# Performance work log

Measured on AMD Instinct MI355X. Metric: run time of the kernel, lower is better.

The kernel has to match this reference:

```python
import jax, jax.numpy as jnp
import numpy as np

B, D, H, L = 2, 1024, 16, 4
BLK = 16                 # block_size == max_text_tokens
MT, MF = 16, 2032        # max_text_tokens, max_font_tokens
S = MT + MF              # 2048
NB = S // BLK            # 128 blocks
V = 490                  # font_vocab_size
HD = D // H              # 64
WIN = 30                 # 3*max_glyph_tokens/block_size = 3*160/16
NGLOB, NRAND = 1, 2      # BigBird global / random blocks
SOS = 0.42


def _make_layout():
    # Deterministic BigBird block layout per head: [H, NB, NB] bool
    rng = np.random.default_rng(0)
    layout = np.zeros((H, NB, NB), dtype=bool)
    layout[:, :NGLOB, :] = True          # global rows
    layout[:, :, :NGLOB] = True          # global cols
    for i in range(NB):                  # sliding window
        layout[:, i, max(0, i - WIN // 2):min(NB, i + WIN // 2 + 1)] = True
    for h in range(H):                   # random blocks
        for i in range(NB):
            layout[h, i, rng.choice(NB, size=NRAND, replace=False)] = True
    return jnp.asarray(layout)


def setup_inputs() -> dict:
    key = jax.random.key(0)
    ks = jax.random.split(key, 16)
    p = lambda k, shape: (0.02 * jax.random.normal(k, shape)).astype(jnp.float32)
    return {
        "text_embeddings": jax.random.normal(ks[0], (B, MT, D), jnp.float32),
        "font_embeddings": jax.random.normal(ks[1], (B, MF, D), jnp.float32),
        "layout": _make_layout(),
        "Wq": p(ks[2], (L, D, D)), "bq": jnp.zeros((L, D), jnp.float32),
        "Wk": p(ks[3], (L, D, D)), "bk": jnp.zeros((L, D), jnp.float32),
        "Wv": p(ks[4], (L, D, D)), "bv": jnp.zeros((L, D), jnp.float32),
        "Wo": p(ks[5], (L, D, D)), "bo": jnp.zeros((L, D), jnp.float32),
        "ln1_g": jnp.ones((L, D), jnp.float32), "ln1_b": jnp.zeros((L, D), jnp.float32),
        "ln2_g": jnp.ones((L, D), jnp.float32), "ln2_b": jnp.zeros((L, D), jnp.float32),
        "W1": p(ks[6], (L, D, 4 * D)), "b1": jnp.zeros((L, 4 * D), jnp.float32),
        "W2": p(ks[7], (L, 4 * D, D)), "b2": jnp.zeros((L, D), jnp.float32),
        "lnf_g": jnp.ones((D,), jnp.float32), "lnf_b": jnp.zeros((D,), jnp.float32),
        "Wout": p(ks[8], (D, V)),
    }


def _ln(x, g, b, eps=1e-5):
    mu = x.mean(-1, keepdims=True)
    var = ((x - mu) ** 2).mean(-1, keepdims=True)
    return (x - mu) * jax.lax.rsqrt(var + eps) * g + b


def _forward(text_embeddings, font_embeddings, layout, Wq, bq, Wk, bk, Wv, bv, Wo, bo,
             ln1_g, ln1_b, ln2_g, ln2_b, W1, b1, W2, b2, lnf_g, lnf_b, Wout):
    sos = jnp.full((B, 1, D), SOS, text_embeddings.dtype)
    x = jnp.concatenate([sos, text_embeddings, font_embeddings[:, :-1, :]], axis=1)  # [B,S,D]
    # token-level mask = block-sparse BigBird layout AND causal -> [H,S,S]
    tok_mask = jnp.repeat(jnp.repeat(layout, BLK, axis=1), BLK, axis=2)
    tok_mask = tok_mask & jnp.tril(jnp.ones((S, S), bool))[None]
    neg = jnp.asarray(-1e9, x.dtype)
    scale = jnp.asarray(1.0 / np.sqrt(HD), x.dtype)

    def layer(x, p):
        wq, bq_, wk, bk_, wv, bv_, wo, bo_, g1, gb1, g2, gb2, w1, bb1, w2, bb2 = p
        q = (x @ wq + bq_).reshape(B, S, H, HD).transpose(0, 2, 1, 3)
        k = (x @ wk + bk_).reshape(B, S, H, HD).transpose(0, 2, 1, 3)
        v = (x @ wv + bv_).reshape(B, S, H, HD).transpose(0, 2, 1, 3)
        scores = jnp.einsum('bhqd,bhkd->bhqk', q, k) * scale
        scores = jnp.where(tok_mask[None], scores, neg)
        probs = jax.nn.softmax(scores, axis=-1)
        a = jnp.einsum('bhqk,bhkd->bhqd', probs, v).transpose(0, 2, 1, 3).reshape(B, S, D)
        a = a @ wo + bo_
        x = _ln(x + a, g1, gb1)                                   # post-norm residual
        m = jax.nn.gelu(x @ w1 + bb1, approximate=False) @ w2 + bb2  # dropout=eval no-op
        x = _ln(x + m, g2, gb2)
        return x, None

    params = (Wq, bq, Wk, bk, Wv, bv, Wo, bo, ln1_g, ln1_b, ln2_g, ln2_b, W1, b1, W2, b2)
    x, _ = jax.lax.scan(jax.checkpoint(layer), x, params)
    logits = _ln(x, lnf_g, lnf_b) @ Wout                          # [B,S,V]
    return logits[:, :MT, :], logits[:, MT:, :]


def reference(text_embeddings, font_embeddings, layout, Wq, bq, Wk, bk, Wv, bv, Wo, bo,
              ln1_g, ln1_b, ln2_g, ln2_b, W1, b1, W2, b2, lnf_g, lnf_b, Wout):
    return _forward(text_embeddings, font_embeddings, layout, Wq, bq, Wk, bk, Wv, bv, Wo, bo,
                    ln1_g, ln1_b, ln2_g, ln2_b, W1, b1, W2, b2, lnf_g, lnf_b, Wout)
```

## Files before the change

### kernel.cpp

```cpp
#include <hip/hip_runtime.h>
#include <hip/hip_bf16.h>
#include <math.h>


typedef __hip_bfloat16 bf16;
typedef __attribute__((ext_vector_type(8))) short bf16x8;
typedef __attribute__((ext_vector_type(8))) unsigned short us8;
typedef __attribute__((ext_vector_type(4))) unsigned short us4;
typedef __attribute__((ext_vector_type(4))) float f32x4;
typedef __attribute__((ext_vector_type(8))) _Float16 f16x8;

#define S_LEN 2048
#define D_MODEL 1024
#define NBLK 128
#define NHEAD 16
#define BATCH 2
#define M_ROWS 4096
#define VOCAB 490

__device__ __forceinline__ float ldw(const void* p, size_t i, bool bf) {
    return bf ? __bfloat162float(((const bf16*)p)[i]) : ((const float*)p)[i];
}
__device__ __forceinline__ bool is_bf(const unsigned* probe) {
    return probe[0] != 0x3F800000u;
}
__device__ __forceinline__ unsigned short f2b(float f) {
    union { float f; unsigned u; } x; x.f = f;
    return (unsigned short)((x.u + 0x7FFFu + ((x.u >> 16) & 1u)) >> 16);
}
__device__ __forceinline__ unsigned short f2h(float f) {
    union { _Float16 h; unsigned short u; } x; x.h = (_Float16)f;
    return x.u;
}
__device__ __forceinline__ unsigned packh(float a, float b) {
    return (unsigned)f2h(a) | ((unsigned)f2h(b) << 16);
}

__global__ __launch_bounds__(256) void norm_layout_kernel(
    const unsigned char* __restrict__ lraw, unsigned char* __restrict__ mask)
{
    int i = blockIdx.x * 256 + threadIdx.x;
    bool bytes_mode = (lraw[1] == 1);
    unsigned char v;
    if (bytes_mode) v = lraw[i] ? 1 : 0;
    else            v = ((const unsigned*)lraw)[i] ? 1 : 0;
    mask[i] = v;
}

__global__ __launch_bounds__(256) void build_x_kernel(
    const void* __restrict__ text, const void* __restrict__ font,
    float* __restrict__ x, unsigned short* __restrict__ xb,
    const unsigned* __restrict__ probe)
{
    bool bf = is_bf(probe);
    size_t idx = (size_t)blockIdx.x * 256 + threadIdx.x;
    int d = (int)(idx & 1023);
    int s = (int)((idx >> 10) & 2047);
    int b = (int)(idx >> 21);
    float v;
    if (s == 0)       v = bf ? 0.419921875f : 0.42f;
    else if (s <= 16) v = ldw(text, ((size_t)(b * 16 + (s - 1))) * 1024 + d, bf);
    else              v = ldw(font, ((size_t)(b * 2032 + (s - 17))) * 1024 + d, bf);
    x[idx] = v;
    xb[idx] = f2b(v);
}

__global__ __launch_bounds__(256) void transw_kernel(
    const void* __restrict__ W, size_t wOff, unsigned short* __restrict__ Wt,
    int K, int N, const unsigned* __restrict__ probe)
{
    bool bf = is_bf(probe);
    __shared__ unsigned short tile[32][34];
    int k0 = blockIdx.x * 32, n0 = blockIdx.y * 32;
    int t = threadIdx.x, c = t & 31, r0 = t >> 5;
    #pragma unroll
    for (int i = 0; i < 4; ++i) {
        int n = n0 + c;
        float v = (n < N) ? ldw(W, wOff + (size_t)(k0 + r0 + i * 8) * N + n, bf) : 0.f;
        tile[r0 + i * 8][c] = f2b(v);
    }
    __syncthreads();
    #pragma unroll
    for (int i = 0; i < 4; ++i)
        Wt[(size_t)(n0 + r0 + i * 8) * K + k0 + c] = tile[c][r0 + i * 8];
}

__global__ __launch_bounds__(256) void transw4_kernel(
    const void* __restrict__ Wa, const void* __restrict__ Wb,
    const void* __restrict__ Wc, const void* __restrict__ Wd,
    size_t wOff, unsigned short* __restrict__ wt,
    const unsigned* __restrict__ probe)
{
    bool bf = is_bf(probe);
    int z = blockIdx.z;
    const void* W = z == 0 ? Wa : (z == 1 ? Wb : (z == 2 ? Wc : Wd));
    unsigned short* Wt = wt + (size_t)z * (1u << 20);
    __shared__ unsigned short tile[32][34];
    int k0 = blockIdx.x * 32, n0 = blockIdx.y * 32;
    int t = threadIdx.x, c = t & 31, r0 = t >> 5;
    #pragma unroll
    for (int i = 0; i < 4; ++i) {
        float v = ldw(W, wOff + (size_t)(k0 + r0 + i * 8) * 1024 + n0 + c, bf);
        tile[r0 + i * 8][c] = f2b(v);
    }
    __syncthreads();
    #pragma unroll
    for (int i = 0; i < 4; ++i)
        Wt[(size_t)(n0 + r0 + i * 8) * 1024 + k0 + c] = tile[c][r0 + i * 8];
}

__global__ __launch_bounds__(512) void gemm_kernel(
    const unsigned short* __restrict__ Ab,
    const unsigned short* __restrict__ Wt, size_t wtStride,
    const void* __restrict__ b0, const void* __restrict__ b1p, const void* __restrict__ b2p,
    size_t bOff,
    float* __restrict__ C0, float* __restrict__ C1, float* __restrict__ C2,
    void* __restrict__ Cb0, void* __restrict__ Cb1, void* __restrict__ Cb2,
    int M, int N, int K, int act, int outmode, const unsigned* __restrict__ probe)
{
    bool bf = is_bf(probe);
    __shared__ __align__(16) unsigned short As[2][128 * 64];
    __shared__ __align__(16) unsigned short Bs[2][128 * 64];

    int t    = threadIdx.x;
    int lane = t & 63;
    int wid  = t >> 6;
    int wm   = wid >> 2;
    int wn   = wid & 3;

    int gx  = gridDim.x;
    int nwg = gx * gridDim.y;
    int bid = blockIdx.y * gx + blockIdx.x;
    int swz = (bid & 7) * (nwg >> 3) + (bid >> 3);
    int m0  = (swz / gx) * 128;
    int n0t = (swz % gx) * 128;
    int sel = n0t / N;
    int n0  = n0t - sel * N;

    const void* bias = sel == 0 ? b0 : (sel == 1 ? b1p : b2p);
    float* C         = sel == 0 ? C0 : (sel == 1 ? C1 : C2);
    void* Cb         = sel == 0 ? Cb0 : (sel == 1 ? Cb1 : Cb2);
    const unsigned short* Wtb = Wt + (size_t)sel * wtStride;

    f32x4 acc[4][2];
    #pragma unroll
    for (int i = 0; i < 4; i++)
        #pragma unroll
        for (int j = 0; j < 2; j++)
            acc[i][j] = (f32x4){0.f, 0.f, 0.f, 0.f};

    const int fm = lane & 15;

    auto stageA = [&](int bb, int kt) {
        int k0 = kt << 6;
        #pragma unroll
        for (int c = 0; c < 2; ++c) {
            int p    = (wid * 2 + c) * 64 + lane;
            int row  = p >> 3;
            int cp   = p & 7;
            int csrc = cp ^ (row & 7);
            const unsigned short* src = Ab + (size_t)(m0 + row) * K + k0 + csrc * 8;
            unsigned short* dst = &As[bb][(wid * 2 + c) * 512];
            __builtin_amdgcn_global_load_lds(
                (const __attribute__((address_space(1))) unsigned int*)src,
                (__attribute__((address_space(3))) unsigned int*)dst, 16, 0, 0);
        }
    };
    auto stageB = [&](int bb, int kt) {
        int k0 = kt << 6;
        #pragma unroll
        for (int c = 0; c < 2; ++c) {
            int p    = (wid * 2 + c) * 64 + lane;
            int row  = p >> 3;
            int cp   = p & 7;
            int csrc = cp ^ (row & 7);
            const unsigned short* src = Wtb + (size_t)(n0 + row) * K + k0 + csrc * 8;
            unsigned short* dst = &Bs[bb][(wid * 2 + c) * 512];
            __builtin_amdgcn_global_load_lds(
                (const __attribute__((address_space(1))) unsigned int*)src,
                (__attribute__((address_space(3))) unsigned int*)dst, 16, 0, 0);
        }
    };
    auto compute = [&](int bb) {
        #pragma unroll
        for (int kk = 0; kk < 2; ++kk) {
            int cq = kk * 4 + (lane >> 4);
            bf16x8 af[4], bfr[2];
            #pragma unroll
            for (int i = 0; i < 4; ++i) {
                int r = wm * 64 + i * 16 + fm;
                af[i] = *(const bf16x8*)(&As[bb][r * 64 + (cq ^ (r & 7)) * 8]);
            }
            #pragma unroll
            for (int j = 0; j < 2; ++j) {
                int n = wn * 32 + j * 16 + fm;
                bfr[j] = *(const bf16x8*)(&Bs[bb][n * 64 + (cq ^ (n & 7)) * 8]);
            }
            #pragma unroll
            for (int i = 0; i < 4; ++i)
                #pragma unroll
                for (int j = 0; j < 2; ++j)
                    acc[i][j] = __builtin_amdgcn_mfma_f32_16x16x32_bf16(
                        af[i], bfr[j], acc[i][j], 0, 0, 0);
        }
    };

    int nt = K >> 6;
    stageA(0, 0);
    stageB(0, 0);
    __syncthreads();

    for (int kt = 0; kt < nt; ++kt) {
        int cur = kt & 1;
        bool more = (kt + 1) < nt;
        if (more) { stageA(cur ^ 1, kt + 1); stageB(cur ^ 1, kt + 1); }
        compute(cur);
        __syncthreads();
    }

    int rq = (lane >> 4) * 4;
    #pragma unroll
    for (int j = 0; j < 2; ++j) {
        int n = n0 + wn * 32 + j * 16 + fm;
        if (n >= N) continue;
        float bv = bias ? ldw(bias, bOff + n, bf) : 0.f;
        #pragma unroll
        for (int i = 0; i < 4; ++i) {
            int mb = m0 + wm * 64 + i * 16 + rq;
            #pragma unroll
            for (int r = 0; r < 4; ++r) {
                int m = mb + r;
                float v = acc[i][j][r] + bv;
                if (act == 1) v = 0.5f * v * (1.f + erff(v * 0.70710678118654752f));
                if (outmode == 0) {
                    C[(size_t)m * N + n] = v;
                } else if (outmode == 2) {
                    ((unsigned short*)Cb)[(size_t)m * N + n] = f2b(v);
                } else if (outmode == 3) {
                    ((unsigned short*)Cb)[(size_t)m * N + n] = f2h(v);
                } else {
                    int b = m >> 11;
                    int s = m & 2047;
                    size_t dst;
                    if (s < 16) dst = ((size_t)(b * 16 + s)) * N + n;
                    else        dst = (size_t)(BATCH * 16) * N + ((size_t)(b * 2032 + (s - 16))) * N + n;
                    if (bf) ((unsigned short*)Cb)[dst] = f2b(v);
                    else    ((float*)Cb)[dst] = v;
                }
            }
        }
    }
}

__global__ __launch_bounds__(256) void attn_kernel(
    const unsigned short* __restrict__ q16, const unsigned short* __restrict__ k16,
    const unsigned short* __restrict__ v16, const unsigned char* __restrict__ mask,
    unsigned short* __restrict__ ab)
{
    int n = blockIdx.x;
    int qgrp = ((n & 7) << 2) | (n >> 3);
    int h = blockIdx.y, b = blockIdx.z;

    __shared__ __align__(16) unsigned short ksd[16][72];
    __shared__ __align__(16) unsigned short vst[64][16];
    __shared__ unsigned char ujn[128];

    int t = threadIdx.x, lane = t & 63, w = t >> 6;
    int qb = qgrp * 4 + w;
    const int fm = lane & 15, rq = lane >> 4;
    int jmax = qgrp * 4 + 3;

    const unsigned char* mrow0 = mask + ((size_t)h * NBLK) * NBLK;
    if (t <= jmax) {
        int j = t;
        unsigned char u = 0;
        #pragma unroll
        for (int ww = 0; ww < 4; ++ww) {
            int qq = qgrp * 4 + ww;
            u |= (unsigned char)((j <= qq) && mrow0[qq * NBLK + j]);
        }
        ujn[j] = u;
    }

    int qrow = qb * 16 + fm;
    size_t qbase = ((size_t)(b * S_LEN + qrow)) * D_MODEL + h * 64;
    f16x8 qf0 = *(const f16x8*)(q16 + qbase + rq * 8);
    f16x8 qf1 = *(const f16x8*)(q16 + qbase + 32 + rq * 8);

    f32x4 O[4];
    #pragma unroll
    for (int c = 0; c < 4; ++c) O[c] = (f32x4){0.f, 0.f, 0.f, 0.f};
    float m_run = -1e30f, l_run = 0.f;
    const f16x8 hzero = (f16x8){0,0,0,0,0,0,0,0};

    __syncthreads();

    int stok = t >> 4, sdg = (t & 15) * 4;
    size_t sbase = ((size_t)(b * S_LEN)) * D_MODEL + h * 64 + sdg;

    for (int j = 0; j <= jmax; ++j) {
        if (!ujn[j]) continue;
        __syncthreads();
        size_t koff = sbase + (size_t)(j * 16 + stok) * D_MODEL;
        us4 kv = *(const us4*)(k16 + koff);
        us4 vv = *(const us4*)(v16 + koff);
        *(us4*)(&ksd[stok][sdg]) = kv;
        vst[sdg + 0][stok] = vv[0]; vst[sdg + 1][stok] = vv[1];
        vst[sdg + 2][stok] = vv[2]; vst[sdg + 3][stok] = vv[3];
        __syncthreads();

        bool active = (j <= qb) && mrow0[qb * NBLK + j];
        if (!active) continue;

        f16x8 kf0 = *(const f16x8*)(&ksd[fm][rq * 8]);
        f16x8 kf1 = *(const f16x8*)(&ksd[fm][32 + rq * 8]);
        f32x4 st = (f32x4){0.f, 0.f, 0.f, 0.f};
        st = __builtin_amdgcn_mfma_f32_16x16x32_f16(kf0, qf0, st, 0, 0, 0);
        st = __builtin_amdgcn_mfma_f32_16x16x32_f16(kf1, qf1, st, 0, 0, 0);

        float s[4];
        #pragma unroll
        for (int r = 0; r < 4; ++r) {
            s[r] = st[r] * 0.125f;
            if (j == qb && (rq * 4 + r) > fm) s[r] = -1e30f;
        }
        float mx = fmaxf(fmaxf(s[0], s[1]), fmaxf(s[2], s[3]));
        mx = fmaxf(mx, __shfl_xor(mx, 16));
        mx = fmaxf(mx, __shfl_xor(mx, 32));
        mx = fmaxf(m_run, mx);
        float al = expf(m_run - mx);
        float p[4]; float ls = 0.f;
        #pragma unroll
        for (int r = 0; r < 4; ++r) {
            p[r] = (s[r] < -1e29f) ? 0.f : expf(s[r] - mx);
            ls += p[r];
        }
        ls += __shfl_xor(ls, 16);
        ls += __shfl_xor(ls, 32);
        l_run = l_run * al + ls;
        m_run = mx;

        unsigned ph01 = packh(p[0], p[1]), ph23 = packh(p[2], p[3]);
        int s0 = fm + (((rq & 1) * 2) << 4);
        int s1 = s0 + 16;
        unsigned w0 = __shfl(ph01, s0), w1 = __shfl(ph23, s0);
        unsigned w2 = __shfl(ph01, s1), w3 = __shfl(ph23, s1);
        union { unsigned u[4]; f16x8 v; } pcv;
        pcv.u[0] = w0; pcv.u[1] = w1; pcv.u[2] = w2; pcv.u[3] = w3;
        f16x8 pa = (rq < 2) ? pcv.v : hzero;

        float al0 = __shfl(al, rq * 4 + 0), al1 = __shfl(al, rq * 4 + 1);
        float al2 = __shfl(al, rq * 4 + 2), al3 = __shfl(al, rq * 4 + 3);
        #pragma unroll
        for (int c = 0; c < 4; ++c) {
            O[c][0] *= al0; O[c][1] *= al1; O[c][2] *= al2; O[c][3] *= al3;
            f16x8 vb = hzero;
            if (rq < 2) vb = *(const f16x8*)(&vst[c * 16 + fm][rq * 8]);
            O[c] = __builtin_amdgcn_mfma_f32_16x16x32_f16(pa, vb, O[c], 0, 0, 0);
        }
    }

    float li0 = 1.f / __shfl(l_run, rq * 4 + 0);
    float li1 = 1.f / __shfl(l_run, rq * 4 + 1);
    float li2 = 1.f / __shfl(l_run, rq * 4 + 2);
    float li3 = 1.f / __shfl(l_run, rq * 4 + 3);
    size_t obase = ((size_t)(b * S_LEN + qb * 16)) * D_MODEL + h * 64;
    #pragma unroll
    for (int c = 0; c < 4; ++c) {
        ab[obase + (size_t)(rq * 4 + 0) * D_MODEL + c * 16 + fm] = f2b(O[c][0] * li0);
        ab[obase + (size_t)(rq * 4 + 1) * D_MODEL + c * 16 + fm] = f2b(O[c][1] * li1);
        ab[obase + (size_t)(rq * 4 + 2) * D_MODEL + c * 16 + fm] = f2b(O[c][2] * li2);
        ab[obase + (size_t)(rq * 4 + 3) * D_MODEL + c * 16 + fm] = f2b(O[c][3] * li3);
    }
}

__global__ __launch_bounds__(256) void add_ln_kernel(
    const float* __restrict__ xin, const float* __restrict__ res,
    float* __restrict__ xout, unsigned short* __restrict__ bfout,
    const void* __restrict__ g, size_t gOff,
    const void* __restrict__ bt, size_t bOff, const unsigned* __restrict__ probe)
{
    bool bf = is_bf(probe);
    int row = blockIdx.x;
    int t = threadIdx.x;
    __shared__ float red[4];

    float4 xv = ((const float4*)(xin + (size_t)row * D_MODEL))[t];
    if (res) {
        float4 rv = ((const float4*)(res + (size_t)row * D_MODEL))[t];
        xv.x += rv.x; xv.y += rv.y; xv.z += rv.z; xv.w += rv.w;
    }
    float s = xv.x + xv.y + xv.z + xv.w;
    for (int off = 32; off > 0; off >>= 1) s += __shfl_down(s, off);
    if ((t & 63) == 0) red[t >> 6] = s;
    __syncthreads();
    float mu = (red[0] + red[1] + red[2] + red[3]) * (1.f / 1024.f);
    __syncthreads();

    float d0 = xv.x - mu, d1 = xv.y - mu, d2 = xv.z - mu, d3 = xv.w - mu;
    float s2 = d0 * d0 + d1 * d1 + d2 * d2 + d3 * d3;
    for (int off = 32; off > 0; off >>= 1) s2 += __shfl_down(s2, off);
    if ((t & 63) == 0) red[t >> 6] = s2;
    __syncthreads();
    float var = (red[0] + red[1] + red[2] + red[3]) * (1.f / 1024.f);
    float rstd = rsqrtf(var + 1e-5f);

    int dbase = t * 4;
    float4 ov;
    ov.x = d0 * rstd * ldw(g, gOff + dbase + 0, bf) + ldw(bt, bOff + dbase + 0, bf);
    ov.y = d1 * rstd * ldw(g, gOff + dbase + 1, bf) + ldw(bt, bOff + dbase + 1, bf);
    ov.z = d2 * rstd * ldw(g, gOff + dbase + 2, bf) + ldw(bt, bOff + dbase + 2, bf);
    ov.w = d3 * rstd * ldw(g, gOff + dbase + 3, bf) + ldw(bt, bOff + dbase + 3, bf);
    ((float4*)(xout + (size_t)row * D_MODEL))[t] = ov;
    if (bfout) {
        us4 bv = { f2b(ov.x), f2b(ov.y), f2b(ov.z), f2b(ov.w) };
        *(us4*)(bfout + (size_t)row * D_MODEL + dbase) = bv;
    }
}

extern "C" void kernel_launch(void* const* d_in, const int* in_sizes, int n_in,
                              void* d_out, int out_size, void* d_ws, size_t ws_size,
                              hipStream_t stream) {
    const void* text  = d_in[0];
    const void* font  = d_in[1];
    const unsigned char* lraw = (const unsigned char*)d_in[2];
    const void* Wq    = d_in[3];
    const void* bq    = d_in[4];
    const void* Wk    = d_in[5];
    const void* bk    = d_in[6];
    const void* Wv    = d_in[7];
    const void* bv    = d_in[8];
    const void* Wo    = d_in[9];
    const void* bo_   = d_in[10];
    const void* ln1g  = d_in[11];
    const void* ln1b  = d_in[12];
    const void* ln2g  = d_in[13];
    const void* ln2b  = d_in[14];
    const void* W1    = d_in[15];
    const void* b1    = d_in[16];
    const void* W2    = d_in[17];
    const void* b2    = d_in[18];
    const void* lnfg  = d_in[19];
    const void* lnfb  = d_in[20];
    const void* Wout  = d_in[21];
    const unsigned* probe = (const unsigned*)d_in[11];

    const size_t Q = (size_t)M_ROWS * D_MODEL;
    float* ws = (float*)d_ws;
    float* x  = ws;
    float* G0 = ws + Q;
    unsigned short* q16 = (unsigned short*)(ws + 2 * Q);
    unsigned short* k16 = q16 + Q;
    unsigned short* v16 = k16 + Q;
    unsigned short* hb  = (unsigned short*)(ws + 2 * Q);
    unsigned short* xb  = (unsigned short*)(ws + 4 * Q);
    unsigned short* ab  = (unsigned short*)(ws + 4 * Q + Q / 2);
    unsigned char* mask = (unsigned char*)(ws + 5 * Q);
    unsigned short* wt  = (unsigned short*)((char*)d_ws + 5 * Q * 4 + 262144);

    norm_layout_kernel<<<(NHEAD * NBLK * NBLK) / 256, 256, 0, stream>>>(lraw, mask);
    build_x_kernel<<<(BATCH * S_LEN * D_MODEL) / 256, 256, 0, stream>>>(text, font, x, xb, probe);

    dim3 gQKV(3 * D_MODEL / 128, M_ROWS / 128);
    dim3 gD(D_MODEL / 128, M_ROWS / 128);
    dim3 gF(4 * D_MODEL / 128, M_ROWS / 128);
    dim3 gV((VOCAB + 127) / 128, M_ROWS / 128);

    const size_t MSZ = (size_t)1 << 20;

    for (int l = 0; l < 4; l++) {
        size_t wo  = (size_t)l * D_MODEL * D_MODEL;
        size_t bo1 = (size_t)l * D_MODEL;
        size_t w1o = (size_t)l * D_MODEL * 4 * D_MODEL;
        size_t b1o = (size_t)l * 4 * D_MODEL;

        transw4_kernel<<<dim3(32, 32, 4), 256, 0, stream>>>(Wq, Wk, Wv, Wo, wo, wt, probe);

        gemm_kernel<<<gQKV, 512, 0, stream>>>(xb, wt, MSZ, bq, bk, bv, bo1,
                                              nullptr, nullptr, nullptr, q16, k16, v16,
                                              M_ROWS, D_MODEL, D_MODEL, 0, 3, probe);
        attn_kernel<<<dim3(S_LEN / 64, NHEAD, BATCH), 256, 0, stream>>>(
            q16, k16, v16, mask, ab);
        gemm_kernel<<<gD, 512, 0, stream>>>(ab, wt + 3 * MSZ, 0, bo_, bo_, bo_, bo1,
                                            G0, G0, G0, nullptr, nullptr, nullptr,
                                            M_ROWS, D_MODEL, D_MODEL, 0, 0, probe);
        add_ln_kernel<<<M_ROWS, 256, 0, stream>>>(x, G0, x, xb, ln1g, bo1, ln1b, bo1, probe);

        transw_kernel<<<dim3(32, 128), 256, 0, stream>>>(W1, w1o, wt, D_MODEL, 4 * D_MODEL, probe);
        transw_kernel<<<dim3(128, 32), 256, 0, stream>>>(W2, w1o, wt + 4 * MSZ, 4 * D_MODEL, D_MODEL, probe);

        gemm_kernel<<<gF, 512, 0, stream>>>(xb, wt, 0, b1, b1, b1, b1o,
                                            nullptr, nullptr, nullptr, hb, hb, hb,
                                            M_ROWS, 4 * D_MODEL, D_MODEL, 1, 2, probe);
        gemm_kernel<<<gD, 512, 0, stream>>>(hb, wt + 4 * MSZ, 0, b2, b2, b2, bo1,
                                            G0, G0, G0, nullptr, nullptr, nullptr,
                                            M_ROWS, D_MODEL, 4 * D_MODEL, 0, 0, probe);
        add_ln_kernel<<<M_ROWS, 256, 0, stream>>>(x, G0, x, xb, ln2g, bo1, ln2b, bo1, probe);
    }

    add_ln_kernel<<<M_ROWS, 256, 0, stream>>>(x, nullptr, G0, ab, lnfg, 0, lnfb, 0, probe);
    transw_kernel<<<dim3(32, 16), 256, 0, stream>>>(Wout, 0, wt, D_MODEL, VOCAB, probe);
    gemm_kernel<<<gV, 512, 0, stream>>>(ab, wt, 0, nullptr, nullptr, nullptr, 0,
                                        nullptr, nullptr, nullptr, d_out, d_out, d_out,
                                        M_ROWS, VOCAB, D_MODEL, 0, 1, probe);
}
```

Measured before the change: 1.508 ms.

## Stage 64-token K/V chunks with prefetch and pre-transposed V in attention

The V projection GEMM epilogue now writes V transposed per (batch, head) as [d][s] in fp16, so the attention kernel can load V rows with wide vector loads instead of scattering a transpose into shared memory. The attention kernel processes keys in 64-token chunks (four 16-token blocks), builds a compact list of active chunks, and register-prefetches the next chunk's K/V while computing the current one. It uses XOR-swizzled LDS layouts to avoid bank conflicts. The aim is fewer barriers and wider global loads, at the cost of loading whole chunks even when only some blocks in them are active and of removing the block-index swizzle.

New measurement: 1.409 ms. -6.6%, faster.

```diff
diff --git a/kernel.cpp b/kernel.cpp
--- a/kernel.cpp
+++ b/kernel.cpp
@@ -141,6 +141,7 @@
     float* C         = sel == 0 ? C0 : (sel == 1 ? C1 : C2);
     void* Cb         = sel == 0 ? Cb0 : (sel == 1 ? Cb1 : Cb2);
     const unsigned short* Wtb = Wt + (size_t)sel * wtStride;
+    const bool vtr = (outmode == 3 && sel == 2);
 
     f32x4 acc[4][2];
     #pragma unroll
@@ -227,6 +228,14 @@
         #pragma unroll
         for (int i = 0; i < 4; ++i) {
             int mb = m0 + wm * 64 + i * 16 + rq;
+            if (vtr) {
+                us4 o;
+                #pragma unroll
+                for (int r = 0; r < 4; ++r) o[r] = f2h(acc[i][j][r] + bv);
+                int bb2 = mb >> 11, s0 = mb & 2047, hh = n >> 6, dd = n & 63;
+                *(us4*)(&((unsigned short*)Cb)[((((size_t)(bb2 * 16 + hh)) * 64 + dd) << 11) + s0]) = o;
+                continue;
+            }
             #pragma unroll
             for (int r = 0; r < 4; ++r) {
                 int m = mb + r;
@@ -254,32 +263,44 @@
 
 __global__ __launch_bounds__(256) void attn_kernel(
     const unsigned short* __restrict__ q16, const unsigned short* __restrict__ k16,
-    const unsigned short* __restrict__ v16, const unsigned char* __restrict__ mask,
+    const unsigned short* __restrict__ v16t, const unsigned char* __restrict__ mask,
     unsigned short* __restrict__ ab)
 {
-    int n = blockIdx.x;
-    int qgrp = ((n & 7) << 2) | (n >> 3);
+    int qgrp = blockIdx.x;
     int h = blockIdx.y, b = blockIdx.z;
 
-    __shared__ __align__(16) unsigned short ksd[16][72];
-    __shared__ __align__(16) unsigned short vst[64][16];
-    __shared__ unsigned char ujn[128];
+    __shared__ __align__(16) unsigned short ksd[64 * 64];
+    __shared__ __align__(16) unsigned short vst[64 * 64];
+    __shared__ unsigned char cflag[33];
+    __shared__ unsigned char aclist[33];
+    __shared__ int nac;
 
     int t = threadIdx.x, lane = t & 63, w = t >> 6;
     int qb = qgrp * 4 + w;
     const int fm = lane & 15, rq = lane >> 4;
-    int jmax = qgrp * 4 + 3;
 
     const unsigned char* mrow0 = mask + ((size_t)h * NBLK) * NBLK;
-    if (t <= jmax) {
-        int j = t;
-        unsigned char u = 0;
-        #pragma unroll
-        for (int ww = 0; ww < 4; ++ww) {
-            int qq = qgrp * 4 + ww;
-            u |= (unsigned char)((j <= qq) && mrow0[qq * NBLK + j]);
+
+    if (t <= qgrp) {
+        int jc = t;
+        bool f = false;
+        #pragma unroll
+        for (int mb = 0; mb < 4; ++mb) {
+            int j = jc * 4 + mb;
+            #pragma unroll
+            for (int ww = 0; ww < 4; ++ww) {
+                int qq = qgrp * 4 + ww;
+                f = f || ((j <= qq) && mrow0[qq * NBLK + j]);
+            }
         }
-        ujn[j] = u;
+        cflag[jc] = f ? 1 : 0;
+    }
+    __syncthreads();
+    if (t == 0) {
+        int n = 0;
+        for (int jc = 0; jc <= qgrp; ++jc)
+            if (cflag[jc]) aclist[n++] = (unsigned char)jc;
+        nac = n;
     }
 
     int qrow = qb * 16 + fm;
@@ -294,69 +315,94 @@
     const f16x8 hzero = (f16x8){0,0,0,0,0,0,0,0};
 
     __syncthreads();
-
-    int stok = t >> 4, sdg = (t & 15) * 4;
-    size_t sbase = ((size_t)(b * S_LEN)) * D_MODEL + h * 64 + sdg;
-
-    for (int j = 0; j <= jmax; ++j) {
-        if (!ujn[j]) continue;
+    int nacl = nac;
+
+    const int srow = t >> 2;
+    const int sg   = (t & 3) * 2;
+    const size_t vtbase = ((size_t)(b * NHEAD + h) * 64) * S_LEN;
+    us8 kr0, kr1, vr0, vr1;
+
+    auto loadKV = [&](int jc) {
+        size_t kb = ((size_t)(b * S_LEN + jc * 64 + srow)) * D_MODEL + h * 64 + sg * 8;
+        kr0 = *(const us8*)(k16 + kb);
+        kr1 = *(const us8*)(k16 + kb + 8);
+        size_t vb_ = vtbase + (size_t)srow * S_LEN + jc * 64 + sg * 8;
+        vr0 = *(const us8*)(v16t + vb_);
+        vr1 = *(const us8*)(v16t + vb_ + 8);
+    };
+    auto writeKV = [&]() {
+        int p0 = (sg) ^ (srow & 7), p1 = (sg + 1) ^ (srow & 7);
+        *(us8*)(&ksd[srow * 64 + p0 * 8]) = kr0;
+        *(us8*)(&ksd[srow * 64 + p1 * 8]) = kr1;
+        *(us8*)(&vst[srow * 64 + p0 * 8]) = vr0;
+        *(us8*)(&vst[srow * 64 + p1 * 8]) = vr1;
+    };
+
+    if (nacl > 0) loadKV(aclist[0]);
+
+    for (int ci = 0; ci < nacl; ++ci) {
+        int jc = aclist[ci];
         __syncthreads();
-        size_t koff = sbase + (size_t)(j * 16 + stok) * D_MODEL;
-        us4 kv = *(const us4*)(k16 + koff);
-        us4 vv = *(const us4*)(v16 + koff);
-        *(us4*)(&ksd[stok][sdg]) = kv;
-        vst[sdg + 0][stok] = vv[0]; vst[sdg + 1][stok] = vv[1];
-        vst[sdg + 2][stok] = vv[2]; vst[sdg + 3][stok] = vv[3];
+        writeKV();
+        if (ci + 1 < nacl) loadKV(aclist[ci + 1]);
         __syncthreads();
 
-        bool active = (j <= qb) && mrow0[qb * NBLK + j];
-        if (!active) continue;
-
-        f16x8 kf0 = *(const f16x8*)(&ksd[fm][rq * 8]);
-        f16x8 kf1 = *(const f16x8*)(&ksd[fm][32 + rq * 8]);
-        f32x4 st = (f32x4){0.f, 0.f, 0.f, 0.f};
-        st = __builtin_amdgcn_mfma_f32_16x16x32_f16(kf0, qf0, st, 0, 0, 0);
-        st = __builtin_amdgcn_mfma_f32_16x16x32_f16(kf1, qf1, st, 0, 0, 0);
-
-        float s[4];
-        #pragma unroll
-        for (int r = 0; r < 4; ++r) {
-            s[r] = st[r] * 0.125f;
-            if (j == qb && (rq * 4 + r) > fm) s[r] = -1e30f;
-        }
-        float mx = fmaxf(fmaxf(s[0], s[1]), fmaxf(s[2], s[3]));
-        mx = fmaxf(mx, __shfl_xor(mx, 16));
-        mx = fmaxf(mx, __shfl_xor(mx, 32));
-        mx = fmaxf(m_run, mx);
-        float al = expf(m_run - mx);
-        float p[4]; float ls = 0.f;
-        #pragma unroll
-        for (int r = 0; r < 4; ++r) {
-            p[r] = (s[r] < -1e29f) ? 0.f : expf(s[r] - mx);
-            ls += p[r];
-        }
-        ls += __shfl_xor(ls, 16);
-        ls += __shfl_xor(ls, 32);
-        l_run = l_run * al + ls;
-        m_run = mx;
-
-        unsigned ph01 = packh(p[0], p[1]), ph23 = packh(p[2], p[3]);
-        int s0 = fm + (((rq & 1) * 2) << 4);
-        int s1 = s0 + 16;
-        unsigned w0 = __shfl(ph01, s0), w1 = __shfl(ph23, s0);
-        unsigned w2 = __shfl(ph01, s1), w3 = __shfl(ph23, s1);
-        union { unsigned u[4]; f16x8 v; } pcv;
-        pcv.u[0] = w0; pcv.u[1] = w1; pcv.u[2] = w2; pcv.u[3] = w3;
-        f16x8 pa = (rq < 2) ? pcv.v : hzero;
-
-        float al0 = __shfl(al, rq * 4 + 0), al1 = __shfl(al, rq * 4 + 1);
-        float al2 = __shfl(al, rq * 4 + 2), al3 = __shfl(al, rq * 4 + 3);
-        #pragma unroll
-        for (int c = 0; c < 4; ++c) {
-            O[c][0] *= al0; O[c][1] *= al1; O[c][2] *= al2; O[c][3] *= al3;
-            f16x8 vb = hzero;
-            if (rq < 2) vb = *(const f16x8*)(&vst[c * 16 + fm][rq * 8]);
-            O[c] = __builtin_amdgcn_mfma_f32_16x16x32_f16(pa, vb, O[c], 0, 0, 0);
+        #pragma unroll
+        for (int mb = 0; mb < 4; ++mb) {
+            int j = jc * 4 + mb;
+            bool actv = (j <= qb) && mrow0[qb * NBLK + j];
+            if (!actv) continue;
+
+            int krow = mb * 16 + fm;
+            f16x8 kf0 = *(const f16x8*)(&ksd[krow * 64 + ((0 * 4 + rq) ^ (krow & 7)) * 8]);
+            f16x8 kf1 = *(const f16x8*)(&ksd[krow * 64 + ((1 * 4 + rq) ^ (krow & 7)) * 8]);
+            f32x4 st = (f32x4){0.f, 0.f, 0.f, 0.f};
+            st = __builtin_amdgcn_mfma_f32_16x16x32_f16(kf0, qf0, st, 0, 0, 0);
+            st = __builtin_amdgcn_mfma_f32_16x16x32_f16(kf1, qf1, st, 0, 0, 0);
+
+            float s[4];
+            #pragma unroll
+            for (int r = 0; r < 4; ++r) {
+                s[r] = st[r] * 0.125f;
+                if (j == qb && (rq * 4 + r) > fm) s[r] = -1e30f;
+            }
+            float mx = fmaxf(fmaxf(s[0], s[1]), fmaxf(s[2], s[3]));
+            mx = fmaxf(mx, __shfl_xor(mx, 16));
+            mx = fmaxf(mx, __shfl_xor(mx, 32));
+            mx = fmaxf(m_run, mx);
+            float al = expf(m_run - mx);
+            float p[4]; float ls = 0.f;
+            #pragma unroll
+            for (int r = 0; r < 4; ++r) {
+                p[r] = (s[r] < -1e29f) ? 0.f : expf(s[r] - mx);
+                ls += p[r];
+            }
+            ls += __shfl_xor(ls, 16);
+            ls += __shfl_xor(ls, 32);
+            l_run = l_run * al + ls;
+            m_run = mx;
+
+            unsigned ph01 = packh(p[0], p[1]), ph23 = packh(p[2], p[3]);
+            int s0 = fm + (((rq & 1) * 2) << 4);
+            int s1 = s0 + 16;
+            unsigned w0 = __shfl(ph01, s0), w1 = __shfl(ph23, s0);
+            unsigned w2 = __shfl(ph01, s1), w3 = __shfl(ph23, s1);
+            union { unsigned u[4]; f16x8 v; } pcv;
+            pcv.u[0] = w0; pcv.u[1] = w1; pcv.u[2] = w2; pcv.u[3] = w3;
+            f16x8 pa = (rq < 2) ? pcv.v : hzero;
+
+            float al0 = __shfl(al, rq * 4 + 0), al1 = __shfl(al, rq * 4 + 1);
+            float al2 = __shfl(al, rq * 4 + 2), al3 = __shfl(al, rq * 4 + 3);
+            #pragma unroll
+            for (int c = 0; c < 4; ++c) {
+                O[c][0] *= al0; O[c][1] *= al1; O[c][2] *= al2; O[c][3] *= al3;
+                f16x8 vb = hzero;
+                if (rq < 2) {
+                    int vrow = c * 16 + fm;
+                    vb = *(const f16x8*)(&vst[vrow * 64 + ((mb * 2 + rq) ^ (vrow & 7)) * 8]);
+                }
+                O[c] = __builtin_amdgcn_mfma_f32_16x16x32_f16(pa, vb, O[c], 0, 0, 0);
+            }
         }
     }
 
```
